# Optimization experiments

Measured on AMD Instinct MI355X. Metric: run time of the kernel, lower is better.

The kernel has to match this reference:

```python
import jax, jax.numpy as jnp
import numpy as np

PAD_token, SOS_token, EOS_token = 0, 1, 2
V, E, H, B, To, Ti = 10000, 512, 512, 32, 256, 1024


def _u(key, shape, fan_in):
    s = 1.0 / np.sqrt(fan_in)
    return jax.random.uniform(key, shape, jnp.float32, -s, s)


def setup_inputs() -> dict:
    key = jax.random.key(0)
    ks = jax.random.split(key, 16)
    inp = {
        "padded_input": jax.random.randint(ks[0], (B, To), 3, V),
        "encoder_padded_outputs": jax.random.normal(ks[1], (B, Ti, H), jnp.float32),
        "embedding": jax.random.normal(ks[2], (V, E), jnp.float32) * 0.02,
        # layer 0 LSTMCell: input = embed + encoder context (E + H)
        "Wih0": _u(ks[3], (4 * H, E + H), H), "Whh0": _u(ks[4], (4 * H, H), H),
        "bih0": _u(ks[5], (4 * H,), H),       "bhh0": _u(ks[6], (4 * H,), H),
        # layer 1 LSTMCell: input = H
        "Wih1": _u(ks[7], (4 * H, H), H),     "Whh1": _u(ks[8], (4 * H, H), H),
        "bih1": _u(ks[9], (4 * H,), H),       "bhh1": _u(ks[10], (4 * H,), H),
        # MLP: Linear(2H -> H), Tanh, Linear(H -> V)
        "W1": _u(ks[11], (H, 2 * H), 2 * H),  "b1": _u(ks[12], (H,), 2 * H),
        "W2": _u(ks[13], (V, H), H),          "b2": _u(ks[14], (V,), H),
    }
    return inp


def _lstm_cell(x, h, c, Wih, Whh, bih, bhh):
    g = x @ Wih.T + bih + h @ Whh.T + bhh            # [B, 4H]
    i, f, gg, o = jnp.split(g, 4, axis=-1)           # torch gate order i,f,g,o
    c2 = jax.nn.sigmoid(f) * c + jax.nn.sigmoid(i) * jnp.tanh(gg)
    h2 = jax.nn.sigmoid(o) * jnp.tanh(c2)
    return h2, c2


def reference(padded_input, encoder_padded_outputs, embedding,
              Wih0, Whh0, bih0, bhh0, Wih1, Whh1, bih1, bhh1,
              W1, b1, W2, b2):
    n = padded_input.shape[0]
    sos = jnp.full((n, 1), SOS_token, padded_input.dtype)
    eos = jnp.full((n, 1), EOS_token, padded_input.dtype)
    ys_in = jnp.concatenate([sos, padded_input], axis=1)   # [B, To+1]
    ys_out = jnp.concatenate([padded_input, eos], axis=1)  # [B, To+1]

    emb = embedding[ys_in]                                 # [B, To+1, E]
    emb_t = jnp.swapaxes(emb, 0, 1)                        # [To+1, B, E]
    enc = encoder_padded_outputs                           # [B, Ti, H]

    h0 = jnp.zeros((n, H), enc.dtype)
    init = (h0, h0, h0, h0, jnp.zeros((n, enc.shape[2]), enc.dtype))

    def step(carry, e_t):
        h_0, c_0, h_1, c_1, att_c = carry
        rnn_in = jnp.concatenate([e_t, att_c], axis=1)
        h_0, c_0 = _lstm_cell(rnn_in, h_0, c_0, Wih0, Whh0, bih0, bhh0)
        h_1, c_1 = _lstm_cell(h_0, h_1, c_1, Wih1, Whh1, bih1, bhh1)
        scores = jnp.einsum('bh,bth->bt', h_1, enc)        # [B, Ti]
        att_w = jax.nn.softmax(scores, axis=-1)
        att_c = jnp.einsum('bt,bth->bh', att_w, enc)       # [B, H]
        mlp_in = jnp.concatenate([h_1, att_c], axis=1)
        logits = jnp.tanh(mlp_in @ W1.T + b1) @ W2.T + b2  # [B, V]
        return (h_0, c_0, h_1, c_1, att_c), logits

    _, y_all = jax.lax.scan(step, init, emb_t)             # [To+1, B, V]
    logits = jnp.swapaxes(y_all, 0, 1).reshape(-1, V)      # [B*(To+1), V]
    labels = ys_out.reshape(-1)
    logp = jax.nn.log_softmax(logits, axis=-1)
    nll = -jnp.take_along_axis(logp, labels[:, None], axis=1)[:, 0]
    mask = (labels != PAD_token).astype(logits.dtype)
    loss = jnp.sum(nll * mask) / jnp.maximum(jnp.sum(mask), 1.0)
    return loss
```

## Files before the change

### kernel.cpp

```cpp
#include <hip/hip_runtime.h>
#include <hip/hip_bf16.h>

#define B_    32
#define TO_   256
#define T_    257
#define H_    512
#define V_    10000
#define TI_   1024
#define NROW_ 8224
#define NB_   256

using f32x4 = __attribute__((ext_vector_type(4))) float;
using s16x8 = __attribute__((ext_vector_type(8))) short;
typedef unsigned long long ull;

struct Ptrs {
  const int* padded;
  const float* enc;
  const float* emb;
  const float *Wih0, *Whh0, *bih0, *bhh0;
  const float *Wih1, *Whh1, *bih1, *bhh1;
  const float *W1, *b1, *W2, *b2;
  float* out;
  unsigned short *mlpin;
  unsigned short *embt;
  unsigned short *tanhv;
  unsigned short *W0c;
  unsigned short *W1c;
  unsigned short *W1b;
  unsigned short *W2b;
  float *bias0c, *bias1c;
  unsigned short *attc;
  float *upart;
  float *zp;
  unsigned short *Xh0;
  unsigned short *Xh1;
  float *Xh1f;
  unsigned *arrX;
  unsigned *arrY;
  unsigned *marr;
  unsigned *larr;
  unsigned *ibar;
  float *rowsum;
  float *lablog;
};

__device__ __forceinline__ unsigned short f2b(float f){
  __hip_bfloat16 h = __float2bfloat16(f);
  unsigned short r; __builtin_memcpy(&r, &h, 2); return r;
}
__device__ __forceinline__ float b2f(unsigned short u){
  unsigned v = ((unsigned)u) << 16; float f; __builtin_memcpy(&f, &v, 4); return f;
}
__device__ __forceinline__ float sigf(float x){ return 1.f / (1.f + expf(-x)); }

__device__ __forceinline__ float aldf(const float* p){
  return __hip_atomic_load(p, __ATOMIC_RELAXED, __HIP_MEMORY_SCOPE_AGENT);
}
__device__ __forceinline__ unsigned aldw(const unsigned* p){
  return __hip_atomic_load(p, __ATOMIC_RELAXED, __HIP_MEMORY_SCOPE_AGENT);
}
__device__ __forceinline__ ull aldu(const ull* p){
  return __hip_atomic_load(p, __ATOMIC_RELAXED, __HIP_MEMORY_SCOPE_AGENT);
}
__device__ __forceinline__ void astf(float* p, float v){
  __hip_atomic_store(p, v, __ATOMIC_RELAXED, __HIP_MEMORY_SCOPE_AGENT);
}
__device__ __forceinline__ void astu(ull* p, ull v){
  __hip_atomic_store(p, v, __ATOMIC_RELAXED, __HIP_MEMORY_SCOPE_AGENT);
}
__device__ __forceinline__ void astw(unsigned* p, unsigned v){
  __hip_atomic_store(p, v, __ATOMIC_RELAXED, __HIP_MEMORY_SCOPE_AGENT);
}
#define DRAIN asm volatile("s_waitcnt vmcnt(0)" ::: "memory")

__device__ __forceinline__ void gbarInit(unsigned* bar){
  DRAIN; __syncthreads();
  if (threadIdx.x < 64){
    const int l = threadIdx.x;
    if (l == 0) astw(bar + blockIdx.x * 4, 1u);
    for (;;){
      unsigned f0 = aldw(bar + (l      ) * 4);
      unsigned f1 = aldw(bar + (l +  64) * 4);
      unsigned f2 = aldw(bar + (l + 128) * 4);
      unsigned f3 = aldw(bar + (l + 192) * 4);
      if (__all((f0 >= 1u) & (f1 >= 1u) & (f2 >= 1u) & (f3 >= 1u))) break;
      __builtin_amdgcn_s_sleep(1);
    }
  }
  __syncthreads();
}

__global__ __launch_bounds__(256) void kprep(Ptrs P){
  const int stride = gridDim.x * blockDim.x;
  const int i0 = blockIdx.x * blockDim.x + threadIdx.x;
  for (int i = i0; i < 128 * 4; i += stride){ P.arrX[i] = 0u; P.arrY[i] = 0u; }
  for (int i = i0; i < 256 * 4; i += stride){ P.marr[i] = 0u; P.ibar[i] = 0u; }
  for (int i = i0; i < 32 * 4; i += stride) P.larr[i] = 0u;
  for (int i = i0; i < T_ * B_ * 512; i += stride){
    int k = i & 511, tb = i >> 9, b = tb & 31, t = tb >> 5;
    int tok = (t == 0) ? 1 : P.padded[b * TO_ + (t - 1)];
    P.embt[i] = f2b(P.emb[(size_t)tok * 512 + k]);
  }
  for (int i = i0; i < 2048 * 1536; i += stride){
    int k = i % 1536, gp = i / 1536;
    int j = gp >> 2, q = gp & 3, g = q * 512 + j;
    float v = (k < 1024) ? P.Wih0[(size_t)g * 1024 + k] : P.Whh0[(size_t)g * 512 + (k - 1024)];
    P.W0c[i] = f2b(v);
  }
  for (int i = i0; i < 2048 * 1024; i += stride){
    int k = i & 1023, gp = i >> 10;
    int j = gp >> 2, q = gp & 3, g = q * 512 + j;
    float v = (k < 512) ? P.Wih1[(size_t)g * 512 + k] : P.Whh1[(size_t)g * 512 + (k - 512)];
    P.W1c[i] = f2b(v);
  }
  for (int i = i0; i < 2048; i += stride){
    int j = i >> 2, q = i & 3, g = q * 512 + j;
    P.bias0c[i] = P.bih0[g] + P.bhh0[g];
    P.bias1c[i] = P.bih1[g] + P.bhh1[g];
  }
  for (int i = i0; i < 512 * 1024; i += stride) P.W1b[i] = f2b(P.W1[i]);
  for (int i = i0; i < NROW_; i += stride) P.rowsum[i] = 0.f;
}

__global__ __launch_bounds__(256) void kprep2(Ptrs P){
  const int stride = gridDim.x * blockDim.x;
  const int i0 = blockIdx.x * blockDim.x + threadIdx.x;
  for (int i = i0; i < V_ * 512; i += stride) P.W2b[i] = f2b(P.W2[i]);
}

__global__ __launch_bounds__(256, 1) void kA(Ptrs P){
  __shared__ __align__(16) unsigned short enc_s[128 * 512];
  __shared__ float h1_s[512];
  __shared__ float w_s[128];
  __shared__ float gate_s[2][32][17];
  __shared__ float h_s[32][4];
  __shared__ float zred[2];
  const int bb = blockIdx.x, tid = threadIdx.x;
  const int b_att = bb >> 3, tc = bb & 7;

  {
    const float* ep = P.enc + ((size_t)b_att * TI_ + (size_t)tc * 128) * H_;
    for (int idx = tid; idx < 128 * 512; idx += 256){
      int r = idx >> 9;
      unsigned byteoff = ((unsigned)idx * 2u) ^ ((unsigned)(r & 7) << 4);
      enc_s[byteoff >> 1] = f2b(ep[idx]);
    }
  }
  {
    int g = bb * 256 + tid;
    if (g < 16384){ astw((unsigned*)P.Xh0 + g, 0u); astw((unsigned*)P.Xh1 + g, 0u); }
    if (g < 32768) astf(P.Xh1f + g, 0.f);
    if (g < 8192)  astw((unsigned*)P.attc + g, 0u);
  }
  gbarInit(P.ibar);

  const int wv = tid >> 6, l = tid & 63, lr = l & 15, lk = l >> 4;
  const int bh = wv & 1, kh = wv >> 1;
  const int batch = bh * 16 + lr;
  const int eidx = tid - 128, eb = eidx >> 2, ejl = eidx & 3;
  const bool isGemm = bb < 128;
  const int rb = bb - 128; const bool isRed = (rb >= 0 && rb < 32);
  float c0r = 0.f, c1r = 0.f;

  for (int t = 0; t < T_; ++t){
    const int p = t & 1, pp = p ^ 1;
    const unsigned tv = (unsigned)t + 1u;
    if (isGemm){
      if (t > 0 && tid < 64){
        const unsigned want = tv - 1u;
        for (;;){
          unsigned f = (tid < 32) ? aldw(P.larr + tid * 4) : want;
          if (__all(f >= want)) break;
          __builtin_amdgcn_s_sleep(1);
        }
      }
      __syncthreads();
      {
        const unsigned short* Brow = P.W0c + (size_t)(bb * 16 + lr) * 1536;
        const unsigned short* Erow = P.embt + ((size_t)t * 32 + batch) * 512;
        const ull* Arow = (const ull*)(P.attc + batch * 512);
        const ull* Hrow = (const ull*)(P.Xh0 + pp * 16384 + batch * 512);
        f32x4 acc = {0.f, 0.f, 0.f, 0.f};
        #pragma unroll
        for (int ks = 0; ks < 8; ++ks){
          const int kb = (kh * 8 + ks) * 32 + lk * 8;
          s16x8 a = *(const s16x8*)(Erow + kb);
          s16x8 b = *(const s16x8*)(Brow + kb);
          acc = __builtin_amdgcn_mfma_f32_16x16x32_bf16(a, b, acc, 0, 0, 0);
        }
        #pragma unroll
        for (int ks = 0; ks < 8; ++ks){
          const int kb = (kh * 8 + ks) * 32 + lk * 8;
          ull d0 = aldu(Arow + (kb >> 2)), d1 = aldu(Arow + (kb >> 2) + 1);
          s16x8 a; __builtin_memcpy(&a, &d0, 8); __builtin_memcpy(((char*)&a) + 8, &d1, 8);
          s16x8 b = *(const s16x8*)(Brow + 512 + kb);
          acc = __builtin_amdgcn_mfma_f32_16x16x32_bf16(a, b, acc, 0, 0, 0);
        }
        #pragma unroll
        for (int ks = 0; ks < 8; ++ks){
          const int kb = (kh * 8 + ks) * 32 + lk * 8;
          ull d0 = aldu(Hrow + (kb >> 2)), d1 = aldu(Hrow + (kb >> 2) + 1);
          s16x8 a; __builtin_memcpy(&a, &d0, 8); __builtin_memcpy(((char*)&a) + 8, &d1, 8);
          s16x8 b = *(const s16x8*)(Brow + 1024 + kb);
          acc = __builtin_amdgcn_mfma_f32_16x16x32_bf16(a, b, acc, 0, 0, 0);
        }
        #pragma unroll
        for (int j = 0; j < 4; ++j) gate_s[kh][bh * 16 + lk * 4 + j][lr] = acc[j];
      }
      __syncthreads();
      if (tid >= 128){
        const float* bs = P.bias0c + bb * 16 + ejl * 4;
        float ii = sigf (gate_s[0][eb][ejl * 4 + 0] + gate_s[1][eb][ejl * 4 + 0] + bs[0]);
        float ff = sigf (gate_s[0][eb][ejl * 4 + 1] + gate_s[1][eb][ejl * 4 + 1] + bs[1]);
        float gg = tanhf(gate_s[0][eb][ejl * 4 + 2] + gate_s[1][eb][ejl * 4 + 2] + bs[2]);
        float oo = sigf (gate_s[0][eb][ejl * 4 + 3] + gate_s[1][eb][ejl * 4 + 3] + bs[3]);
        float cn = ff * c0r + ii * gg; c0r = cn;
        h_s[eb][ejl] = oo * tanhf(cn);
      }
      __syncthreads();
      if (tid < 32){
        unsigned short hb[4];
        #pragma unroll
        for (int jl = 0; jl < 4; ++jl) hb[jl] = f2b(h_s[tid][jl]);
        ull v; __builtin_memcpy(&v, hb, 8);
        astu((ull*)(P.Xh0 + p * 16384 + tid * 512 + bb * 4), v);
      }
      DRAIN; __syncthreads();
      if (tid < 64){
        if (tid == 0) astw(P.arrX + bb * 4, tv);
        for (;;){
          unsigned f0 = aldw(P.arrX + tid * 4), f1 = aldw(P.arrX + (tid + 64) * 4);
          if (__all((f0 >= tv) & (f1 >= tv))) break;
          __builtin_amdgcn_s_sleep(1);
        }
      }
      __syncthreads();
      {
        const unsigned short* Brow = P.W1c + (size_t)(bb * 16 + lr) * 1024;
        const ull* H0r = (const ull*)(P.Xh0 + p * 16384 + batch * 512);
        const ull* H1r = (const ull*)(P.Xh1 + pp * 16384 + batch * 512);
        f32x4 acc = {0.f, 0.f, 0.f, 0.f};
        #pragma unroll
        for (int ks = 0; ks < 8; ++ks){
          const int kb = (kh * 8 + ks) * 32 + lk * 8;
          ull d0 = aldu(H0r + (kb >> 2)), d1 = aldu(H0r + (kb >> 2) + 1);
          s16x8 a; __builtin_memcpy(&a, &d0, 8); __builtin_memcpy(((char*)&a) + 8, &d1, 8);
          s16x8 b = *(const s16x8*)(Brow + kb);
          acc = __builtin_amdgcn_mfma_f32_16x16x32_bf16(a, b, acc, 0, 0, 0);
        }
        #pragma unroll
        for (int ks = 0; ks < 8; ++ks){
          const int kb = (kh * 8 + ks) * 32 + lk * 8;
          ull d0 = aldu(H1r + (kb >> 2)), d1 = aldu(H1r + (kb >> 2) + 1);
          s16x8 a; __builtin_memcpy(&a, &d0, 8); __builtin_memcpy(((char*)&a) + 8, &d1, 8);
          s16x8 b = *(const s16x8*)(Brow + 512 + kb);
          acc = __builtin_amdgcn_mfma_f32_16x16x32_bf16(a, b, acc, 0, 0, 0);
        }
        #pragma unroll
        for (int j = 0; j < 4; ++j) gate_s[kh][bh * 16 + lk * 4 + j][lr] = acc[j];
      }
      __syncthreads();
      if (tid >= 128){
        const float* bs = P.bias1c + bb * 16 + ejl * 4;
        float ii = sigf (gate_s[0][eb][ejl * 4 + 0] + gate_s[1][eb][ejl * 4 + 0] + bs[0]);
        float ff = sigf (gate_s[0][eb][ejl * 4 + 1] + gate_s[1][eb][ejl * 4 + 1] + bs[1]);
        float gg = tanhf(gate_s[0][eb][ejl * 4 + 2] + gate_s[1][eb][ejl * 4 + 2] + bs[2]);
        float oo = sigf (gate_s[0][eb][ejl * 4 + 3] + gate_s[1][eb][ejl * 4 + 3] + bs[3]);
        float cn = ff * c1r + ii * gg; c1r = cn;
        h_s[eb][ejl] = oo * tanhf(cn);
      }
      __syncthreads();
      if (tid < 32){
        unsigned short hb[4];
        #pragma unroll
        for (int jl = 0; jl < 4; ++jl) hb[jl] = f2b(h_s[tid][jl]);
        ull vb; __builtin_memcpy(&vb, hb, 8);
        astu((ull*)(P.Xh1 + p * 16384 + tid * 512 + bb * 4), vb);
        *(ull*)(P.mlpin + ((size_t)t * 32 + tid) * 1024 + bb * 4) = vb;
        ull w0, w1;
        __builtin_memcpy(&w0, &h_s[tid][0], 8);
        __builtin_memcpy(&w1, &h_s[tid][2], 8);
        ull* dst = (ull*)P.Xh1f + ((p * 16384 + tid * 512 + bb * 4) >> 1);
        astu(dst, w0); astu(dst + 1, w1);
      }
      DRAIN; __syncthreads();
      if (tid == 0) astw(P.arrY + bb * 4, tv);
    }
    if (tid < 64){
      for (;;){
        unsigned f0 = aldw(P.arrY + tid * 4), f1 = aldw(P.arrY + (tid + 64) * 4);
        if (__all((f0 >= tv) & (f1 >= tv))) break;
        __builtin_amdgcn_s_sleep(1);
      }
    }
    __syncthreads();
    {
      ull v = aldu((const ull*)(P.Xh1f + p * 16384 + b_att * 512) + tid);
      float f2[2]; __builtin_memcpy(f2, &v, 8);
      h1_s[tid * 2] = f2[0]; h1_s[tid * 2 + 1] = f2[1];
    }
    __syncthreads();
    {
      const int ti_l = tid >> 1, half = tid & 1;
      float s = 0.f;
      const unsigned swz = (unsigned)(ti_l & 7) << 4;
      for (int h8 = half * 256; h8 < half * 256 + 256; h8 += 8){
        unsigned byteoff = ((unsigned)(ti_l * 512 + h8) * 2u) ^ swz;
        s16x8 ev = *(const s16x8*)((const char*)enc_s + byteoff);
        #pragma unroll
        for (int e = 0; e < 8; ++e) s += b2f((unsigned short)ev[e]) * h1_s[h8 + e];
      }
      s += __shfl_xor(s, 1);
      if (half == 0) w_s[ti_l] = expf(s);
    }
    __syncthreads();
    {
      if (tid < 128){
        float z = w_s[tid];
        #pragma unroll
        for (int off = 1; off < 64; off <<= 1) z += __shfl_xor(z, off);
        if ((tid & 63) == 0) zred[tid >> 6] = z;
      }
      float a0 = 0.f, a1 = 0.f;
      const int hc = tid * 2;
      for (int ti = 0; ti < 128; ++ti){
        const float wvv = w_s[ti];
        unsigned byteoff = ((unsigned)(ti * 1024 + hc * 2)) ^ ((unsigned)(ti & 7) << 4);
        unsigned pk = *(const unsigned*)((const char*)enc_s + byteoff);
        a0 += wvv * b2f((unsigned short)(pk & 0xffffu));
        a1 += wvv * b2f((unsigned short)(pk >> 16));
      }
      float f2[2] = {a0, a1};
      ull pv; __builtin_memcpy(&pv, f2, 8);
      astu((ull*)(P.upart + ((size_t)b_att * 8 + tc) * 512 + hc), pv);
      __syncthreads();
      if (tid == 0) astf(P.zp + b_att * 8 + tc, zred[0] + zred[1]);
      DRAIN; __syncthreads();
      if (tid == 0) astw(P.marr + (b_att * 8 + tc) * 4, tv);
    }
    if (isRed){
      if (tid < 64){
        for (;;){
          unsigned f = (tid < 8) ? aldw(P.marr + (rb * 8 + tid) * 4) : tv;
          if (__all(f >= tv)) break;
          __builtin_amdgcn_s_sleep(1);
        }
      }
      __syncthreads();
      const int hc = tid * 2;
      float s0 = 0.f, s1 = 0.f, zs = 0.f;
      #pragma unroll
      for (int c = 0; c < 8; ++c){
        ull v = aldu((const ull*)(P.upart + ((size_t)rb * 8 + c) * 512 + hc));
        float f2[2]; __builtin_memcpy(f2, &v, 8);
        s0 += f2[0]; s1 += f2[1];
        zs += aldf(P.zp + rb * 8 + c);
      }
      const float rZ = 1.f / zs;
      unsigned pk = (unsigned)f2b(s0 * rZ) | ((unsigned)f2b(s1 * rZ) << 16);
      astw(((unsigned*)P.attc) + rb * 256 + tid, pk);
      *(unsigned*)(P.mlpin + ((size_t)t * 32 + rb) * 1024 + 512 + hc) = pk;
      DRAIN; __syncthreads();
      if (tid == 0) astw(P.larr + rb * 4, tv);
    }
  }
}

__global__ __launch_bounds__(256) void kB1(Ptrs P){
  const int wid = blockIdx.x * 4 + (threadIdx.x >> 6);
  if (wid >= 129 * 8) return;
  const int mt = wid >> 3, nt = wid & 7;
  const int l = threadIdx.x & 63, lr = l & 15, lk = l >> 4;
  const int mr = mt * 64, nc = nt * 64;
  f32x4 acc[4][4] = {};
  for (int k0 = 0; k0 < 1024; k0 += 32){
    s16x8 af[4], bfm[4];
    #pragma unroll
    for (int f = 0; f < 4; ++f){
      int row = mr + f * 16 + lr; if (row > NROW_ - 1) row = NROW_ - 1;
      af[f] = *(const s16x8*)(P.mlpin + (size_t)row * 1024 + k0 + lk * 8);
      int col = nc + f * 16 + lr;
      bfm[f] = *(const s16x8*)(P.W1b + (size_t)col * 1024 + k0 + lk * 8);
    }
    #pragma unroll
    for (int fi = 0; fi < 4; ++fi)
      #pragma unroll
      for (int fj = 0; fj < 4; ++fj)
        acc[fi][fj] = __builtin_amdgcn_mfma_f32_16x16x32_bf16(af[fi], bfm[fj], acc[fi][fj], 0, 0, 0);
  }
  #pragma unroll
  for (int fi = 0; fi < 4; ++fi){
    #pragma unroll
    for (int jj = 0; jj < 4; ++jj){
      int m = mr + fi * 16 + lk * 4 + jj;
      if (m >= NROW_) continue;
      #pragma unroll
      for (int fj = 0; fj < 4; ++fj){
        int n = nc + fj * 16 + lr;
        P.tanhv[(size_t)m * 512 + n] = f2b(tanhf(acc[fi][fj][jj] + P.b1[n]));
      }
    }
  }
}

__global__ __launch_bounds__(256) void kB2(Ptrs P){
  const int wid = blockIdx.x * 4 + (threadIdx.x >> 6);
  if (wid >= 129 * 157) return;
  const int mt = wid / 157, nt = wid % 157;
  const int l = threadIdx.x & 63, lr = l & 15, lk = l >> 4;
  const int mr = mt * 64, nc = nt * 64;
  f32x4 acc[4][4] = {};
  for (int k0 = 0; k0 < 512; k0 += 32){
    s16x8 af[4], bfm[4];
    #pragma unroll
    for (int f = 0; f < 4; ++f){
      int row = mr + f * 16 + lr; if (row > NROW_ - 1) row = NROW_ - 1;
      af[f] = *(const s16x8*)(P.tanhv + (size_t)row * 512 + k0 + lk * 8);
      int col = nc + f * 16 + lr; if (col > V_ - 1) col = V_ - 1;
      bfm[f] = *(const s16x8*)(P.W2b + (size_t)col * 512 + k0 + lk * 8);
    }
    #pragma unroll
    for (int fi = 0; fi < 4; ++fi)
      #pragma unroll
      for (int fj = 0; fj < 4; ++fj)
        acc[fi][fj] = __builtin_amdgcn_mfma_f32_16x16x32_bf16(af[fi], bfm[fj], acc[fi][fj], 0, 0, 0);
  }
  #pragma unroll
  for (int fi = 0; fi < 4; ++fi){
    #pragma unroll
    for (int jj = 0; jj < 4; ++jj){
      const int m = mr + fi * 16 + lk * 4 + jj;
      float s = 0.f;
      #pragma unroll
      for (int fj = 0; fj < 4; ++fj){
        int n = nc + fj * 16 + lr;
        if (n < V_) s += expf(acc[fi][fj][jj] + P.b2[n]);
      }
      s += __shfl_xor(s, 1); s += __shfl_xor(s, 2);
      s += __shfl_xor(s, 4); s += __shfl_xor(s, 8);
      if (lr == 0 && m < NROW_) unsafeAtomicAdd(P.rowsum + m, s);
    }
  }
}

__global__ __launch_bounds__(256) void kL1(Ptrs P){
  const int wid = blockIdx.x * 4 + (threadIdx.x >> 6);
  if (wid >= NROW_) return;
  const int l = threadIdx.x & 63;
  const int t = wid >> 5, b = wid & 31;
  const int lab = (t < TO_) ? P.padded[b * TO_ + t] : 2;
  float s = 0.f;
  s16x8 av = *(const s16x8*)(P.tanhv + (size_t)wid * 512 + l * 8);
  s16x8 wv = *(const s16x8*)(P.W2b + (size_t)lab * 512 + l * 8);
  #pragma unroll
  for (int e = 0; e < 8; ++e) s += b2f((unsigned short)av[e]) * b2f((unsigned short)wv[e]);
  #pragma unroll
  for (int off = 1; off < 64; off <<= 1) s += __shfl_xor(s, off);
  if (l == 0) P.lablog[wid] = s + P.b2[lab];
}

__global__ __launch_bounds__(512) void kL2(Ptrs P){
  __shared__ float ssum[8], scnt[8];
  const int tid = threadIdx.x;
  float sum = 0.f, cnt = 0.f;
  for (int r = tid; r < NROW_; r += 512){
    int t = r >> 5, b = r & 31;
    int lab = (t < TO_) ? P.padded[b * TO_ + t] : 2;
    if (lab != 0){ sum += logf(P.rowsum[r]) - P.lablog[r]; cnt += 1.f; }
  }
  #pragma unroll
  for (int off = 1; off < 64; off <<= 1){ sum += __shfl_xor(sum, off); cnt += __shfl_xor(cnt, off); }
  if ((tid & 63) == 0){ ssum[tid >> 6] = sum; scnt[tid >> 6] = cnt; }
  __syncthreads();
  if (tid == 0){
    float S = 0.f, C = 0.f;
    for (int i = 0; i < 8; ++i){ S += ssum[i]; C += scnt[i]; }
    P.out[0] = S / fmaxf(C, 1.f);
  }
}

extern "C" void kernel_launch(void* const* d_in, const int* in_sizes, int n_in,
                              void* d_out, int out_size, void* d_ws, size_t ws_size,
                              hipStream_t stream){
  (void)in_sizes; (void)n_in; (void)out_size; (void)ws_size;
  Ptrs P;
  P.padded = (const int*)d_in[0];
  P.enc    = (const float*)d_in[1];
  P.emb    = (const float*)d_in[2];
  P.Wih0 = (const float*)d_in[3];  P.Whh0 = (const float*)d_in[4];
  P.bih0 = (const float*)d_in[5];  P.bhh0 = (const float*)d_in[6];
  P.Wih1 = (const float*)d_in[7];  P.Whh1 = (const float*)d_in[8];
  P.bih1 = (const float*)d_in[9];  P.bhh1 = (const float*)d_in[10];
  P.W1 = (const float*)d_in[11];   P.b1 = (const float*)d_in[12];
  P.W2 = (const float*)d_in[13];   P.b2 = (const float*)d_in[14];
  P.out = (float*)d_out;

  char* w = (char*)d_ws;
  size_t off = 0;
  auto take = [&](size_t bytes) -> void* {
    void* ptr = (void*)(w + off);
    off += (bytes + 255) & ~(size_t)255;
    return ptr;
  };
  P.mlpin  = (unsigned short*)take((size_t)T_ * B_ * 1024 * 2);
  P.embt   = (unsigned short*)take((size_t)T_ * B_ * 512 * 2);
  P.tanhv  = P.embt;
  P.W0c    = (unsigned short*)take((size_t)2048 * 1536 * 2);
  P.W1c    = (unsigned short*)take((size_t)2048 * 1024 * 2);
  P.W2b    = P.W0c;
  P.W1b    = (unsigned short*)take((size_t)512 * 1024 * 2);
  P.bias0c = (float*)take(2048 * 4);
  P.bias1c = (float*)take(2048 * 4);
  P.attc   = (unsigned short*)take(32 * 512 * 2);
  P.upart  = (float*)take((size_t)32 * 8 * 512 * 4);
  P.zp     = (float*)take(32 * 8 * 4);
  P.Xh0    = (unsigned short*)take(2 * 32 * 512 * 2);
  P.Xh1    = (unsigned short*)take(2 * 32 * 512 * 2);
  P.Xh1f   = (float*)take(2 * 32 * 512 * 4);
  P.arrX   = (unsigned*)take(128 * 4 * 4);
  P.arrY   = (unsigned*)take(128 * 4 * 4);
  P.marr   = (unsigned*)take(256 * 4 * 4);
  P.larr   = (unsigned*)take(32 * 4 * 4);
  P.ibar   = (unsigned*)take(256 * 4 * 4);
  P.rowsum = (float*)take(NROW_ * 4);
  P.lablog = (float*)take(NROW_ * 4);

  kprep<<<dim3(2048), dim3(256), 0, stream>>>(P);
  void* args[] = { (void*)&P };
  hipLaunchCooperativeKernel(kA, dim3(NB_), dim3(256), args, 0, stream);
  kprep2<<<dim3(1024), dim3(256), 0, stream>>>(P);
  kB1<<<dim3(258),  dim3(256), 0, stream>>>(P);
  kB2<<<dim3(5064), dim3(256), 0, stream>>>(P);
  kL1<<<dim3(2056), dim3(256), 0, stream>>>(P);
  kL2<<<dim3(1),    dim3(512), 0, stream>>>(P);
}
```

Measured before the change: 7.714 ms.

## Replace attention reduction stage with atomic accumulation and overlap embedding GEMM with wait

Drops the dedicated reduction blocks and the larr barrier. Attention blocks now atomically add their partial context vectors and softmax denominators into double-buffered u/Zb arrays, and the gate GEMM normalizes u by Z on the fly. The embedding and recurrent-h parts of the layer-0 GEMM are issued before waiting on the attention flags, so they overlap with the attention stage. Other blocks zero the next buffers and write mlpin columns. The change also adds spin caps on every barrier, which can silently break synchronization if a wait ever takes too long, and it makes the float atomic accumulation order nondeterministic.

```diff
diff --git a/kernel.cpp b/kernel.cpp
--- a/kernel.cpp
+++ b/kernel.cpp
@@ -9,6 +9,7 @@
 #define TI_   1024
 #define NROW_ 8224
 #define NB_   256
+#define SPINCAP 150000
 
 using f32x4 = __attribute__((ext_vector_type(4))) float;
 using s16x8 = __attribute__((ext_vector_type(8))) short;
@@ -30,16 +31,14 @@
   unsigned short *W1b;
   unsigned short *W2b;
   float *bias0c, *bias1c;
-  unsigned short *attc;
-  float *upart;
-  float *zp;
+  float *u;
+  float *Zb;
   unsigned short *Xh0;
   unsigned short *Xh1;
   float *Xh1f;
   unsigned *arrX;
   unsigned *arrY;
   unsigned *marr;
-  unsigned *larr;
   unsigned *ibar;
   float *rowsum;
   float *lablog;
@@ -79,12 +78,14 @@
   if (threadIdx.x < 64){
     const int l = threadIdx.x;
     if (l == 0) astw(bar + blockIdx.x * 4, 1u);
+    int spin = 0;
     for (;;){
       unsigned f0 = aldw(bar + (l      ) * 4);
       unsigned f1 = aldw(bar + (l +  64) * 4);
       unsigned f2 = aldw(bar + (l + 128) * 4);
       unsigned f3 = aldw(bar + (l + 192) * 4);
       if (__all((f0 >= 1u) & (f1 >= 1u) & (f2 >= 1u) & (f3 >= 1u))) break;
+      if (++spin > SPINCAP) break;
       __builtin_amdgcn_s_sleep(1);
     }
   }
@@ -94,9 +95,8 @@
 __global__ __launch_bounds__(256) void kprep(Ptrs P){
   const int stride = gridDim.x * blockDim.x;
   const int i0 = blockIdx.x * blockDim.x + threadIdx.x;
-  for (int i = i0; i < 128 * 4; i += stride){ P.arrX[i] = 0u; P.arrY[i] = 0u; }
-  for (int i = i0; i < 256 * 4; i += stride){ P.marr[i] = 0u; P.ibar[i] = 0u; }
-  for (int i = i0; i < 32 * 4; i += stride) P.larr[i] = 0u;
+  for (int i = i0; i < 128 * 4; i += stride) P.arrX[i] = 0u;
+  for (int i = i0; i < 256 * 4; i += stride){ P.arrY[i] = 0u; P.marr[i] = 0u; P.ibar[i] = 0u; }
   for (int i = i0; i < T_ * B_ * 512; i += stride){
     int k = i & 511, tb = i >> 9, b = tb & 31, t = tb >> 5;
     int tok = (t == 0) ? 1 : P.padded[b * TO_ + (t - 1)];
@@ -142,16 +142,16 @@
   {
     const float* ep = P.enc + ((size_t)b_att * TI_ + (size_t)tc * 128) * H_;
     for (int idx = tid; idx < 128 * 512; idx += 256){
-      int r = idx >> 9;
-      unsigned byteoff = ((unsigned)idx * 2u) ^ ((unsigned)(r & 7) << 4);
+      int row = idx >> 9;
+      unsigned byteoff = ((unsigned)idx * 2u) ^ ((unsigned)(row & 7) << 4);
       enc_s[byteoff >> 1] = f2b(ep[idx]);
     }
   }
   {
     int g = bb * 256 + tid;
+    if (g < 32768){ astf(P.u + g, 0.f); astf(P.Xh1f + g, 0.f); }
     if (g < 16384){ astw((unsigned*)P.Xh0 + g, 0u); astw((unsigned*)P.Xh1 + g, 0u); }
-    if (g < 32768) astf(P.Xh1f + g, 0.f);
-    if (g < 8192)  astw((unsigned*)P.attc + g, 0u);
+    if (g < 64) astf(P.Zb + g, (g >= 32) ? 1.f : 0.f);
   }
   gbarInit(P.ibar);
 
@@ -160,43 +160,24 @@
   const int batch = bh * 16 + lr;
   const int eidx = tid - 128, eb = eidx >> 2, ejl = eidx & 3;
   const bool isGemm = bb < 128;
-  const int rb = bb - 128; const bool isRed = (rb >= 0 && rb < 32);
   float c0r = 0.f, c1r = 0.f;
 
   for (int t = 0; t < T_; ++t){
     const int p = t & 1, pp = p ^ 1;
     const unsigned tv = (unsigned)t + 1u;
     if (isGemm){
-      if (t > 0 && tid < 64){
-        const unsigned want = tv - 1u;
-        for (;;){
-          unsigned f = (tid < 32) ? aldw(P.larr + tid * 4) : want;
-          if (__all(f >= want)) break;
-          __builtin_amdgcn_s_sleep(1);
-        }
-      }
-      __syncthreads();
+      const unsigned short* Brow = P.W0c + (size_t)(bb * 16 + lr) * 1536;
+      const unsigned short* Erow = P.embt + ((size_t)t * 32 + batch) * 512;
+      f32x4 acc = {0.f, 0.f, 0.f, 0.f};
+      #pragma unroll
+      for (int ks = 0; ks < 8; ++ks){
+        const int kb = (kh * 8 + ks) * 32 + lk * 8;
+        s16x8 a = *(const s16x8*)(Erow + kb);
+        s16x8 b = *(const s16x8*)(Brow + kb);
+        acc = __builtin_amdgcn_mfma_f32_16x16x32_bf16(a, b, acc, 0, 0, 0);
+      }
       {
-        const unsigned short* Brow = P.W0c + (size_t)(bb * 16 + lr) * 1536;
-        const unsigned short* Erow = P.embt + ((size_t)t * 32 + batch) * 512;
-        const ull* Arow = (const ull*)(P.attc + batch * 512);
         const ull* Hrow = (const ull*)(P.Xh0 + pp * 16384 + batch * 512);
-        f32x4 acc = {0.f, 0.f, 0.f, 0.f};
-        #pragma unroll
-        for (int ks = 0; ks < 8; ++ks){
-          const int kb = (kh * 8 + ks) * 32 + lk * 8;
-          s16x8 a = *(const s16x8*)(Erow + kb);
-          s16x8 b = *(const s16x8*)(Brow + kb);
-          acc = __builtin_amdgcn_mfma_f32_16x16x32_bf16(a, b, acc, 0, 0, 0);
-        }
-        #pragma unroll
-        for (int ks = 0; ks < 8; ++ks){
-          const int kb = (kh * 8 + ks) * 32 + lk * 8;
-          ull d0 = aldu(Arow + (kb >> 2)), d1 = aldu(Arow + (kb >> 2) + 1);
-          s16x8 a; __builtin_memcpy(&a, &d0, 8); __builtin_memcpy(((char*)&a) + 8, &d1, 8);
-          s16x8 b = *(const s16x8*)(Brow + 512 + kb);
-          acc = __builtin_amdgcn_mfma_f32_16x16x32_bf16(a, b, acc, 0, 0, 0);
-        }
         #pragma unroll
         for (int ks = 0; ks < 8; ++ks){
           const int kb = (kh * 8 + ks) * 32 + lk * 8;
@@ -205,9 +186,44 @@
           s16x8 b = *(const s16x8*)(Brow + 1024 + kb);
           acc = __builtin_amdgcn_mfma_f32_16x16x32_bf16(a, b, acc, 0, 0, 0);
         }
-        #pragma unroll
-        for (int j = 0; j < 4; ++j) gate_s[kh][bh * 16 + lk * 4 + j][lr] = acc[j];
-      }
+      }
+      if (t > 0){
+        if (tid < 64){
+          const unsigned want = (unsigned)t;
+          int spin = 0;
+          for (;;){
+            unsigned f0 = aldw(P.marr + (tid      ) * 4);
+            unsigned f1 = aldw(P.marr + (tid +  64) * 4);
+            unsigned f2 = aldw(P.marr + (tid + 128) * 4);
+            unsigned f3 = aldw(P.marr + (tid + 192) * 4);
+            if (__all((f0 >= want) & (f1 >= want) & (f2 >= want) & (f3 >= want))) break;
+            if (++spin > SPINCAP) break;
+            __builtin_amdgcn_s_sleep(1);
+          }
+        }
+        __syncthreads();
+      }
+      {
+        const float* Urow = P.u + pp * 16384 + batch * 512;
+        const float rZ = 1.f / aldf(P.Zb + pp * 32 + batch);
+        #pragma unroll
+        for (int ks = 0; ks < 8; ++ks){
+          const int kb = (kh * 8 + ks) * 32 + lk * 8;
+          ull dd[4];
+          dd[0] = aldu((const ull*)(Urow + kb));
+          dd[1] = aldu((const ull*)(Urow + kb + 2));
+          dd[2] = aldu((const ull*)(Urow + kb + 4));
+          dd[3] = aldu((const ull*)(Urow + kb + 6));
+          float uf[8]; __builtin_memcpy(uf, dd, 32);
+          s16x8 a;
+          #pragma unroll
+          for (int e = 0; e < 8; ++e) a[e] = (short)f2b(uf[e] * rZ);
+          s16x8 b = *(const s16x8*)(Brow + 512 + kb);
+          acc = __builtin_amdgcn_mfma_f32_16x16x32_bf16(a, b, acc, 0, 0, 0);
+        }
+      }
+      #pragma unroll
+      for (int j = 0; j < 4; ++j) gate_s[kh][bh * 16 + lk * 4 + j][lr] = acc[j];
       __syncthreads();
       if (tid >= 128){
         const float* bs = P.bias0c + bb * 16 + ejl * 4;
@@ -227,38 +243,40 @@
         astu((ull*)(P.Xh0 + p * 16384 + tid * 512 + bb * 4), v);
       }
       DRAIN; __syncthreads();
+      if (tid == 0) astw(P.arrX + bb * 4, tv);
       if (tid < 64){
-        if (tid == 0) astw(P.arrX + bb * 4, tv);
+        int spin = 0;
         for (;;){
           unsigned f0 = aldw(P.arrX + tid * 4), f1 = aldw(P.arrX + (tid + 64) * 4);
           if (__all((f0 >= tv) & (f1 >= tv))) break;
+          if (++spin > SPINCAP) break;
           __builtin_amdgcn_s_sleep(1);
         }
       }
       __syncthreads();
       {
-        const unsigned short* Brow = P.W1c + (size_t)(bb * 16 + lr) * 1024;
+        const unsigned short* Brow1 = P.W1c + (size_t)(bb * 16 + lr) * 1024;
         const ull* H0r = (const ull*)(P.Xh0 + p * 16384 + batch * 512);
         const ull* H1r = (const ull*)(P.Xh1 + pp * 16384 + batch * 512);
-        f32x4 acc = {0.f, 0.f, 0.f, 0.f};
+        f32x4 acc2 = {0.f, 0.f, 0.f, 0.f};
         #pragma unroll
         for (int ks = 0; ks < 8; ++ks){
           const int kb = (kh * 8 + ks) * 32 + lk * 8;
           ull d0 = aldu(H0r + (kb >> 2)), d1 = aldu(H0r + (kb >> 2) + 1);
           s16x8 a; __builtin_memcpy(&a, &d0, 8); __builtin_memcpy(((char*)&a) + 8, &d1, 8);
-          s16x8 b = *(const s16x8*)(Brow + kb);
-          acc = __builtin_amdgcn_mfma_f32_16x16x32_bf16(a, b, acc, 0, 0, 0);
+          s16x8 b = *(const s16x8*)(Brow1 + kb);
+          acc2 = __builtin_amdgcn_mfma_f32_16x16x32_bf16(a, b, acc2, 0, 0, 0);
         }
         #pragma unroll
         for (int ks = 0; ks < 8; ++ks){
           const int kb = (kh * 8 + ks) * 32 + lk * 8;
           ull d0 = aldu(H1r + (kb >> 2)), d1 = aldu(H1r + (kb >> 2) + 1);
           s16x8 a; __builtin_memcpy(&a, &d0, 8); __builtin_memcpy(((char*)&a) + 8, &d1, 8);
-          s16x8 b = *(const s16x8*)(Brow + 512 + kb);
-          acc = __builtin_amdgcn_mfma_f32_16x16x32_bf16(a, b, acc, 0, 0, 0);
-        }
-        #pragma unroll
-        for (int j = 0; j < 4; ++j) gate_s[kh][bh * 16 + lk * 4 + j][lr] = acc[j];
+          s16x8 b = *(const s16x8*)(Brow1 + 512 + kb);
+          acc2 = __builtin_amdgcn_mfma_f32_16x16x32_bf16(a, b, acc2, 0, 0, 0);
+        }
+        #pragma unroll
+        for (int j = 0; j < 4; ++j) gate_s[kh][bh * 16 + lk * 4 + j][lr] = acc2[j];
       }
       __syncthreads();
       if (tid >= 128){
@@ -277,7 +295,6 @@
         for (int jl = 0; jl < 4; ++jl) hb[jl] = f2b(h_s[tid][jl]);
         ull vb; __builtin_memcpy(&vb, hb, 8);
         astu((ull*)(P.Xh1 + p * 16384 + tid * 512 + bb * 4), vb);
-        *(ull*)(P.mlpin + ((size_t)t * 32 + tid) * 1024 + bb * 4) = vb;
         ull w0, w1;
         __builtin_memcpy(&w0, &h_s[tid][0], 8);
         __builtin_memcpy(&w1, &h_s[tid][2], 8);
@@ -286,11 +303,56 @@
       }
       DRAIN; __syncthreads();
       if (tid == 0) astw(P.arrY + bb * 4, tv);
+      if (tid < 32){
+        unsigned short hb[4];
+        #pragma unroll
+        for (int jl = 0; jl < 4; ++jl) hb[jl] = f2b(h_s[tid][jl]);
+        ull vb; __builtin_memcpy(&vb, hb, 8);
+        *(ull*)(P.mlpin + ((size_t)t * 32 + tid) * 1024 + bb * 4) = vb;
+      }
+    } else if (bb < 160){
+      if (t > 0){
+        const int b = bb - 128;
+        if (tid < 64){
+          const unsigned want = (unsigned)t;
+          int spin = 0;
+          for (;;){
+            unsigned f = (tid < 8) ? aldw(P.marr + (b * 8 + tid) * 4) : want;
+            if (__all(f >= want)) break;
+            if (++spin > SPINCAP) break;
+            __builtin_amdgcn_s_sleep(1);
+          }
+        }
+        __syncthreads();
+        const float rZ = 1.f / aldf(P.Zb + pp * 32 + b);
+        ull v = aldu((const ull*)(P.u + pp * 16384 + b * 512) + tid);
+        float f2[2]; __builtin_memcpy(f2, &v, 8);
+        unsigned pk = (unsigned)f2b(f2[0] * rZ) | ((unsigned)f2b(f2[1] * rZ) << 16);
+        *(unsigned*)(P.mlpin + ((size_t)(t - 1) * 32 + b) * 1024 + 512 + tid * 2) = pk;
+        DRAIN;
+      }
+      __syncthreads();
+      if (tid == 0) astw(P.arrY + bb * 4, tv);
+    } else if (bb < 224){
+      astf(P.u + p * 16384 + (bb - 160) * 256 + tid, 0.f);
+      DRAIN; __syncthreads();
+      if (tid == 0) astw(P.arrY + bb * 4, tv);
+    } else if (bb == 224){
+      if (tid < 32) astf(P.Zb + p * 32 + tid, 0.f);
+      DRAIN; __syncthreads();
+      if (tid == 0) astw(P.arrY + bb * 4, tv);
+    } else {
+      if (tid == 0) astw(P.arrY + bb * 4, tv);
     }
     if (tid < 64){
+      int spin = 0;
       for (;;){
-        unsigned f0 = aldw(P.arrY + tid * 4), f1 = aldw(P.arrY + (tid + 64) * 4);
-        if (__all((f0 >= tv) & (f1 >= tv))) break;
+        unsigned f0 = aldw(P.arrY + (tid      ) * 4);
+        unsigned f1 = aldw(P.arrY + (tid +  64) * 4);
+        unsigned f2 = aldw(P.arrY + (tid + 128) * 4);
+        unsigned f3 = aldw(P.arrY + (tid + 192) * 4);
+        if (__all((f0 >= tv) & (f1 >= tv) & (f2 >= tv) & (f3 >= tv))) break;
+        if (++spin > SPINCAP) break;
         __builtin_amdgcn_s_sleep(1);
       }
     }
@@ -331,39 +393,32 @@
         a0 += wvv * b2f((unsigned short)(pk & 0xffffu));
         a1 += wvv * b2f((unsigned short)(pk >> 16));
       }
-      float f2[2] = {a0, a1};
-      ull pv; __builtin_memcpy(&pv, f2, 8);
-      astu((ull*)(P.upart + ((size_t)b_att * 8 + tc) * 512 + hc), pv);
-      __syncthreads();
-      if (tid == 0) astf(P.zp + b_att * 8 + tc, zred[0] + zred[1]);
+      unsafeAtomicAdd(P.u + p * 16384 + b_att * 512 + hc, a0);
+      unsafeAtomicAdd(P.u + p * 16384 + b_att * 512 + hc + 1, a1);
+      __syncthreads();
+      if (tid == 0) unsafeAtomicAdd(P.Zb + p * 32 + b_att, zred[0] + zred[1]);
       DRAIN; __syncthreads();
       if (tid == 0) astw(P.marr + (b_att * 8 + tc) * 4, tv);
     }
-    if (isRed){
-      if (tid < 64){
-        for (;;){
-          unsigned f = (tid < 8) ? aldw(P.marr + (rb * 8 + tid) * 4) : tv;
-          if (__all(f >= tv)) break;
-          __builtin_amdgcn_s_sleep(1);
-        }
-      }
-      __syncthreads();
-      const int hc = tid * 2;
-      float s0 = 0.f, s1 = 0.f, zs = 0.f;
-      #pragma unroll
-      for (int c = 0; c < 8; ++c){
-        ull v = aldu((const ull*)(P.upart + ((size_t)rb * 8 + c) * 512 + hc));
-        float f2[2]; __builtin_memcpy(f2, &v, 8);
-        s0 += f2[0]; s1 += f2[1];
-        zs += aldf(P.zp + rb * 8 + c);
-      }
-      const float rZ = 1.f / zs;
-      unsigned pk = (unsigned)f2b(s0 * rZ) | ((unsigned)f2b(s1 * rZ) << 16);
-      astw(((unsigned*)P.attc) + rb * 256 + tid, pk);
-      *(unsigned*)(P.mlpin + ((size_t)t * 32 + rb) * 1024 + 512 + hc) = pk;
-      DRAIN; __syncthreads();
-      if (tid == 0) astw(P.larr + rb * 4, tv);
-    }
+  }
+  if (bb >= 128 && bb < 160){
+    const int b = bb - 128;
+    if (tid < 64){
+      const unsigned want = (unsigned)T_;
+      int spin = 0;
+      for (;;){
+        unsigned f = (tid < 8) ? aldw(P.marr + (b * 8 + tid) * 4) : want;
+        if (__all(f >= want)) break;
+        if (++spin > SPINCAP) break;
+        __builtin_amdgcn_s_sleep(1);
+      }
+    }
+    __syncthreads();
+    const float rZ = 1.f / aldf(P.Zb + 0 * 32 + b);
+    ull v = aldu((const ull*)(P.u + 0 * 16384 + b * 512) + tid);
+    float f2[2]; __builtin_memcpy(f2, &v, 8);
+    unsigned pk = (unsigned)f2b(f2[0] * rZ) | ((unsigned)f2b(f2[1] * rZ) << 16);
+    *(unsigned*)(P.mlpin + ((size_t)256 * 32 + b) * 1024 + 512 + tid * 2) = pk;
   }
 }
 
@@ -464,10 +519,10 @@
   __shared__ float ssum[8], scnt[8];
   const int tid = threadIdx.x;
   float sum = 0.f, cnt = 0.f;
-  for (int r = tid; r < NROW_; r += 512){
-    int t = r >> 5, b = r & 31;
+  for (int rr = tid; rr < NROW_; rr += 512){
+    int t = rr >> 5, b = rr & 31;
     int lab = (t < TO_) ? P.padded[b * TO_ + t] : 2;
-    if (lab != 0){ sum += logf(P.rowsum[r]) - P.lablog[r]; cnt += 1.f; }
+    if (lab != 0){ sum += logf(P.rowsum[rr]) - P.lablog[rr]; cnt += 1.f; }
   }
   #pragma unroll
   for (int off = 1; off < 64; off <<= 1){ sum += __shfl_xor(sum, off); cnt += __shfl_xor(cnt, off); }
@@ -512,16 +567,14 @@
   P.W1b    = (unsigned short*)take((size_t)512 * 1024 * 2);
   P.bias0c = (float*)take(2048 * 4);
   P.bias1c = (float*)take(2048 * 4);
-  P.attc   = (unsigned short*)take(32 * 512 * 2);
-  P.upart  = (float*)take((size_t)32 * 8 * 512 * 4);
-  P.zp     = (float*)take(32 * 8 * 4);
+  P.u      = (float*)take(2 * 32 * 512 * 4);
+  P.Zb     = (float*)take(2 * 32 * 4);
   P.Xh0    = (unsigned short*)take(2 * 32 * 512 * 2);
   P.Xh1    = (unsigned short*)take(2 * 32 * 512 * 2);
   P.Xh1f   = (float*)take(2 * 32 * 512 * 4);
   P.arrX   = (unsigned*)take(128 * 4 * 4);
-  P.arrY   = (unsigned*)take(128 * 4 * 4);
+  P.arrY   = (unsigned*)take(256 * 4 * 4);
   P.marr   = (unsigned*)take(256 * 4 * 4);
-  P.larr   = (unsigned*)take(32 * 4 * 4);
   P.ibar   = (unsigned*)take(256 * 4 * 4);
   P.rowsum = (float*)take(NROW_ * 4);
   P.lablog = (float*)take(NROW_ * 4);
```

New measurement: 7.798 ms. No clear change (+1.1%).
